# Optimization experiments

Measured on AMD Instinct MI355X. Metric: run time of the kernel, lower is better.

The kernel has to match this reference:

```python
import jax, jax.numpy as jnp
import numpy as np

N_NODES = 10000
N_EDGES = 160000
NEG_SLOPE = 0.2


def setup_inputs() -> dict:
    key = jax.random.key(0)
    ks = jax.random.split(key, 24)

    def rn(k, shape, scale):
        return (jax.random.normal(k, shape, dtype=jnp.float32) * scale)

    inp = {
        "x": rn(ks[0], (N_NODES, 128), 1.0),
        "edge_index": jax.random.randint(ks[1], (2, N_EDGES), 0, N_NODES, dtype=jnp.int32),
        "edge_attr": rn(ks[2], (N_EDGES, 8), 1.0),
        # GATConv 1: 128 -> 64 (heads=1)
        "W1": rn(ks[3], (128, 64), 0.09), "as1": rn(ks[4], (64,), 0.1), "ad1": rn(ks[5], (64,), 0.1), "b1": rn(ks[6], (64,), 0.01),
        # GATConv 2: 64 -> 256
        "W2": rn(ks[7], (64, 256), 0.125), "as2": rn(ks[8], (256,), 0.06), "ad2": rn(ks[9], (256,), 0.06), "b2": rn(ks[10], (256,), 0.01),
        # GATConv 3: 256 -> 1024
        "W3": rn(ks[11], (256, 1024), 0.0625), "as3": rn(ks[12], (1024,), 0.03), "ad3": rn(ks[13], (1024,), 0.03), "b3": rn(ks[14], (1024,), 0.01),
        # Dense head
        "lw1": rn(ks[15], (1024, 512), 0.03), "lb1": rn(ks[16], (512,), 0.01),
        "lw2": rn(ks[17], (512, 10), 0.04), "lb2": rn(ks[18], (10,), 0.01),
    }
    return inp


def gat_layer(x, src, dst, W, a_s, a_d, b, n):
    """PyG GATConv, heads=1, concat=True, add_self_loops handled by caller via src/dst."""
    h = x @ W                                   # [N, F_out]
    e = jax.nn.leaky_relu((h @ a_s)[src] + (h @ a_d)[dst], NEG_SLOPE)  # [E']
    m = jax.ops.segment_max(e, dst, num_segments=n)
    ex = jnp.exp(e - m[dst])
    denom = jax.ops.segment_sum(ex, dst, num_segments=n)
    alpha = ex / denom[dst]                     # scatter-softmax over incoming edges
    out = jax.ops.segment_sum(alpha[:, None] * h[src], dst, num_segments=n)
    return out + b


def reference(x, edge_index, edge_attr, W1, as1, ad1, b1, W2, as2, ad2, b2,
              W3, as3, ad3, b3, lw1, lb1, lw2, lb2):
    # edge_attr is accepted but ignored (GATConv built without edge_dim)
    n = x.shape[0]
    loops = jnp.arange(n, dtype=edge_index.dtype)  # add_self_loops=True
    src = jnp.concatenate([edge_index[0], loops])
    dst = jnp.concatenate([edge_index[1], loops])

    h = jax.nn.relu(gat_layer(x, src, dst, W1, as1, ad1, b1, n))
    h = jax.nn.relu(gat_layer(h, src, dst, W2, as2, ad2, b2, n))
    h = jax.nn.relu(gat_layer(h, src, dst, W3, as3, ad3, b3, n))

    pooled = jnp.max(h, axis=0, keepdims=True)  # global_max_pool, batch=None -> [1, 1024]
    z = jax.nn.relu(pooled @ lw1 + lb1)
    z = z @ lw2 + lb2
    return jax.nn.log_softmax(z, axis=1)
```

## Files before the change

kernel.cpp:

```cpp
#include <hip/hip_runtime.h>
#include <hip/hip_bf16.h>
#include <math.h>

#define NEG_SLOPE 0.2f
typedef unsigned short u16;
typedef short bf16x8 __attribute__((ext_vector_type(8)));
typedef float f32x4 __attribute__((ext_vector_type(4)));

__device__ __forceinline__ float bfu2f(u16 u) { return __uint_as_float(((unsigned)u) << 16); }
__device__ __forceinline__ u16 f2bu(float v) { return __bfloat16_as_ushort(__float2bfloat16(v)); }

__device__ __forceinline__ void gload_lds16(const void* g, void* l) {
    __builtin_amdgcn_global_load_lds((const __attribute__((address_space(1))) void*)g,
                                     (__attribute__((address_space(3))) void*)l, 16, 0, 0);
}

__global__ void prep_kernel(int* deg, int* cursor, float* pooled, int N,
                            const float* __restrict__ x, u16* __restrict__ xb,
                            const float* __restrict__ W1, u16* __restrict__ Wt1,
                            const float* __restrict__ W2, u16* __restrict__ Wt2,
                            const float* __restrict__ W3, u16* __restrict__ Wt3,
                            const float* __restrict__ as2, const float* __restrict__ ad2,
                            const float* __restrict__ as3, const float* __restrict__ ad3,
                            float* __restrict__ ws2, float* __restrict__ wd2,
                            float* __restrict__ ws3, float* __restrict__ wd3,
                            int c0, int c1, int c2, int c3, int c4) {
    int bid = blockIdx.x, tid = threadIdx.x;
    if (bid < c0) {
        int i = bid * 256 + tid;
        if (i < N) { deg[i] = 0; cursor[i] = 0; }
        if (i < 1024) pooled[i] = 0.f;
    } else if (bid < c1) {
        int i = (bid - c0) * 256 + tid;
        if (i < N * 128) xb[i] = f2bu(x[i]);
    } else if (bid < c2) {
        int i = (bid - c1) * 256 + tid;
        int k = i % 128, f = i / 128;
        Wt1[i] = f2bu(W1[k * 64 + f]);
    } else if (bid < c3) {
        int i = (bid - c2) * 256 + tid;
        int k = i % 64, f = i / 64;
        Wt2[i] = f2bu(W2[k * 256 + f]);
    } else if (bid < c4) {
        int i = (bid - c3) * 256 + tid;
        int k = i % 256, f = i / 256;
        Wt3[i] = f2bu(W3[(size_t)k * 1024 + f]);
    } else {
        int wv = ((bid - c4) * 256 + tid) >> 6;
        int lane = tid & 63;
        const float *W, *va, *vd; float *os, *od; int F, row;
        if (wv < 64) { W = W2; va = as2; vd = ad2; F = 256; row = wv; os = ws2; od = wd2; }
        else if (wv < 320) { W = W3; va = as3; vd = ad3; F = 1024; row = wv - 64; os = ws3; od = wd3; }
        else return;
        const float* wr = W + (size_t)row * F;
        float ss = 0.f, dd = 0.f;
        for (int f = lane; f < F; f += 64) { float wvv = wr[f]; ss += wvv * va[f]; dd += wvv * vd[f]; }
        for (int off = 32; off; off >>= 1) { ss += __shfl_xor(ss, off); dd += __shfl_xor(dd, off); }
        if (lane == 0) { os[row] = ss; od[row] = dd; }
    }
}

__global__ void count_kernel(const int* __restrict__ edst, int E, int N, int* deg) {
    int i = blockIdx.x * blockDim.x + threadIdx.x;
    int total = E + N;
    if (i >= total) return;
    int dn = (i < E) ? edst[i] : (i - E);
    atomicAdd(&deg[dn], 1);
}

__global__ void scan_kernel(const int* __restrict__ deg, int N, int* __restrict__ offsets) {
    __shared__ int part[257];
    int tid = threadIdx.x;
    int chunk = (N + 255) / 256;
    int begin = tid * chunk;
    int fin = begin + chunk; if (fin > N) fin = N; if (begin > N) begin = N;
    int sum = 0;
    for (int i = begin; i < fin; ++i) sum += deg[i];
    part[tid] = sum;
    __syncthreads();
    if (tid == 0) {
        int acc = 0;
        for (int t = 0; t < 256; ++t) { int v = part[t]; part[t] = acc; acc += v; }
        part[256] = acc;
    }
    __syncthreads();
    int acc = part[tid];
    for (int i = begin; i < fin; ++i) { offsets[i] = acc; acc += deg[i]; }
    if (tid == 255) offsets[N] = part[256];
}

__global__ void scatter_kernel(const int* __restrict__ esrc, const int* __restrict__ edst,
                               int E, int N, const int* __restrict__ offsets,
                               int* cursor, int* __restrict__ srcg) {
    int i = blockIdx.x * blockDim.x + threadIdx.x;
    int total = E + N;
    if (i >= total) return;
    int sn, dn;
    if (i < E) { sn = esrc[i]; dn = edst[i]; } else { sn = i - E; dn = i - E; }
    int pos = atomicAdd(&cursor[dn], 1);
    srcg[offsets[dn] + pos] = sn;
}

template <int K, int MR, bool BIASRELU, bool SD_EPI>
__global__ __launch_bounds__(256) void mfma_gemm(const u16* __restrict__ A,
                                                 const u16* __restrict__ Wt,
                                                 u16* __restrict__ C,
                                                 const float* __restrict__ bias,
                                                 int M, int F,
                                                 const float* __restrict__ asv,
                                                 const float* __restrict__ adv,
                                                 float* __restrict__ s_out,
                                                 float* __restrict__ d_out) {
    constexpr int NK = K / 32;
    int tid = threadIdx.x;
    int w = tid >> 6, l = tid & 63;
    int l15 = l & 15, q = l >> 4;
    int bm = blockIdx.x * (64 * MR);
    int bn = blockIdx.y * 64;
    int r0 = bm + w * (16 * MR);

    const u16* aptr[MR];
    int row[MR];
#pragma unroll
    for (int mr = 0; mr < MR; ++mr) {
        int r = r0 + mr * 16 + l15;
        row[mr] = r;
        int ar = (r < M) ? r : (M - 1);
        aptr[mr] = A + (size_t)ar * K + 8 * q;
    }
    const u16* bptr[4];
#pragma unroll
    for (int nt = 0; nt < 4; ++nt)
        bptr[nt] = Wt + (size_t)(bn + nt * 16 + l15) * K + 8 * q;

    f32x4 acc[MR][4];
#pragma unroll
    for (int mr = 0; mr < MR; ++mr)
#pragma unroll
        for (int nt = 0; nt < 4; ++nt) acc[mr][nt] = (f32x4){0.f, 0.f, 0.f, 0.f};

    bf16x8 a_cur[MR], b_cur[4], a_nxt[MR], b_nxt[4];
#pragma unroll
    for (int mr = 0; mr < MR; ++mr) a_cur[mr] = *(const bf16x8*)(aptr[mr]);
#pragma unroll
    for (int nt = 0; nt < 4; ++nt) b_cur[nt] = *(const bf16x8*)(bptr[nt]);

#pragma unroll
    for (int kk = 0; kk < NK; ++kk) {
        if (kk + 1 < NK) {
            int koff = (kk + 1) * 32;
#pragma unroll
            for (int mr = 0; mr < MR; ++mr) a_nxt[mr] = *(const bf16x8*)(aptr[mr] + koff);
#pragma unroll
            for (int nt = 0; nt < 4; ++nt) b_nxt[nt] = *(const bf16x8*)(bptr[nt] + koff);
        }
#pragma unroll
        for (int mr = 0; mr < MR; ++mr)
#pragma unroll
            for (int nt = 0; nt < 4; ++nt)
                acc[mr][nt] = __builtin_amdgcn_mfma_f32_16x16x32_bf16(b_cur[nt], a_cur[mr], acc[mr][nt], 0, 0, 0);
        if (kk + 1 < NK) {
#pragma unroll
            for (int mr = 0; mr < MR; ++mr) a_cur[mr] = a_nxt[mr];
#pragma unroll
            for (int nt = 0; nt < 4; ++nt) b_cur[nt] = b_nxt[nt];
        }
    }

#pragma unroll
    for (int mr = 0; mr < MR; ++mr) {
        if (row[mr] >= M) continue;
#pragma unroll
        for (int nt = 0; nt < 4; ++nt) {
            int col = bn + nt * 16 + 4 * q;
            ushort4 st;
#pragma unroll
            for (int r = 0; r < 4; ++r) {
                float v = acc[mr][nt][r];
                if (BIASRELU) { v += bias[col + r]; v = fmaxf(v, 0.f); }
                ((u16*)&st)[r] = f2bu(v);
            }
            *(ushort4*)(C + (size_t)row[mr] * F + col) = st;
        }
    }

    if constexpr (SD_EPI) {
        float ss = 0.f, dd = 0.f;
#pragma unroll
        for (int nt = 0; nt < 4; ++nt)
#pragma unroll
            for (int r = 0; r < 4; ++r) {
                int col = nt * 16 + 4 * q + r;
                float v = acc[0][nt][r];
                ss += v * asv[col];
                dd += v * adv[col];
            }
        ss += __shfl_xor(ss, 16); ss += __shfl_xor(ss, 32);
        dd += __shfl_xor(dd, 16); dd += __shfl_xor(dd, 32);
        if (q == 0 && row[0] < M) { s_out[row[0]] = ss; d_out[row[0]] = dd; }
    }
}

__global__ __launch_bounds__(512) void gemm3_kernel(const u16* __restrict__ A,
                                                    const u16* __restrict__ Wt,
                                                    const float* __restrict__ bias,
                                                    int M,
                                                    float* __restrict__ pmaxbuf) {
    constexpr int K = 256;
    constexpr int ABYTES = 128 * 512;
    __shared__ char lds[2 * ABYTES];
    int tid = threadIdx.x;
    int w = tid >> 6, lane = tid & 63;
    int w2 = w >> 2, wc = w & 3;
    int l15 = lane & 15, q = lane >> 4;
    int bid = blockIdx.x;
    int rb = bid >> 2, cbp = bid & 3;
    int bm = rb * 128;

#pragma unroll
    for (int it = 0; it < 8; ++it) {
        int c = it * 512 + tid;
        int row = c >> 5, kc = c & 31;
        int arow = bm + row; if (arow >= M) arow = M - 1;
        gload_lds16(A + (size_t)arow * K + ((kc ^ (row & 7)) * 8),
                    lds + (size_t)(it * 512 + (tid & ~63)) * 16);
    }

    const char* abase = lds;
    char* bldst = lds + ABYTES;

    for (int half = 0; half < 2; ++half) {
        if (half) __syncthreads();
        int bn = cbp * 256 + half * 128;
#pragma unroll
        for (int it = 0; it < 8; ++it) {
            int c = it * 512 + tid;
            int col = c >> 5, kc = c & 31;
            gload_lds16(Wt + (size_t)(bn + col) * K + ((kc ^ (col & 7)) * 8),
                        bldst + (size_t)(it * 512 + (tid & ~63)) * 16);
        }
        __syncthreads();

        f32x4 acc[4][2];
#pragma unroll
        for (int mr = 0; mr < 4; ++mr)
#pragma unroll
            for (int nt = 0; nt < 2; ++nt) acc[mr][nt] = (f32x4){0.f, 0.f, 0.f, 0.f};

        const char* bbase = bldst;
#pragma unroll
        for (int kk = 0; kk < 8; ++kk) {
            int c = kk * 4 + q;
            bf16x8 af[4], bfr[2];
#pragma unroll
            for (int mr = 0; mr < 4; ++mr) {
                int row = w2 * 64 + mr * 16 + l15;
                af[mr] = *(const bf16x8*)(abase + row * 512 + ((c ^ (row & 7)) * 16));
            }
#pragma unroll
            for (int nt = 0; nt < 2; ++nt) {
                int col = wc * 32 + nt * 16 + l15;
                bfr[nt] = *(const bf16x8*)(bbase + col * 512 + ((c ^ (col & 7)) * 16));
            }
#pragma unroll
            for (int mr = 0; mr < 4; ++mr)
#pragma unroll
                for (int nt = 0; nt < 2; ++nt)
                    acc[mr][nt] = __builtin_amdgcn_mfma_f32_16x16x32_bf16(bfr[nt], af[mr], acc[mr][nt], 0, 0, 0);
        }

        float pmax[2][4];
#pragma unroll
        for (int nt = 0; nt < 2; ++nt)
#pragma unroll
            for (int r = 0; r < 4; ++r) pmax[nt][r] = 0.f;
#pragma unroll
        for (int mr = 0; mr < 4; ++mr) {
            bool valid = (bm + w2 * 64 + mr * 16 + l15) < M;
#pragma unroll
            for (int nt = 0; nt < 2; ++nt)
#pragma unroll
                for (int r = 0; r < 4; ++r) {
                    float v = acc[mr][nt][r] + bias[bn + wc * 32 + nt * 16 + 4 * q + r];
                    v = fmaxf(v, 0.f);
                    if (valid) pmax[nt][r] = fmaxf(pmax[nt][r], v);
                }
        }
#pragma unroll
        for (int nt = 0; nt < 2; ++nt)
#pragma unroll
            for (int r = 0; r < 4; ++r) {
#pragma unroll
                for (int msk = 1; msk < 16; msk <<= 1)
                    pmax[nt][r] = fmaxf(pmax[nt][r], __shfl_xor(pmax[nt][r], msk));
            }
        if (l15 == 0) {
#pragma unroll
            for (int nt = 0; nt < 2; ++nt)
#pragma unroll
                for (int r = 0; r < 4; ++r)
                    pmaxbuf[(size_t)(rb * 2 + w2) * 1024 + bn + wc * 32 + nt * 16 + 4 * q + r] = pmax[nt][r];
        }
    }
}

__global__ void sd_kernel(const u16* __restrict__ h, const float* __restrict__ a_s,
                          const float* __restrict__ a_d, int N, int F,
                          float* __restrict__ s, float* __restrict__ d) {
    int wave = (blockIdx.x * blockDim.x + threadIdx.x) >> 6;
    int lane = threadIdx.x & 63;
    if (wave >= N) return;
    const u16* hrow = h + (size_t)wave * F;
    float ss = 0.f, dd = 0.f;
    for (int f = lane * 4; f < F; f += 256) {
        ushort4 u = *reinterpret_cast<const ushort4*>(hrow + f);
        float4 av = *reinterpret_cast<const float4*>(a_s + f);
        float4 dv = *reinterpret_cast<const float4*>(a_d + f);
        float h0 = bfu2f(u.x), h1 = bfu2f(u.y), h2 = bfu2f(u.z), h3 = bfu2f(u.w);
        ss += h0 * av.x + h1 * av.y + h2 * av.z + h3 * av.w;
        dd += h0 * dv.x + h1 * dv.y + h2 * dv.z + h3 * dv.w;
    }
    for (int off = 32; off; off >>= 1) { ss += __shfl_xor(ss, off); dd += __shfl_xor(dd, off); }
    if (lane == 0) { s[wave] = ss; d[wave] = dd; }
}

template <int F, int FS, bool BIASRELU, bool SD_EPI>
__global__ __launch_bounds__(256) void agg_kernel(const u16* __restrict__ h,
                                                  const float* __restrict__ sv,
                                                  const float* __restrict__ dvec,
                                                  const int* __restrict__ srcg,
                                                  const int* __restrict__ offsets,
                                                  const float* __restrict__ bias,
                                                  u16* __restrict__ out,
                                                  const float* __restrict__ wsv,
                                                  const float* __restrict__ wdv,
                                                  float* __restrict__ s_out,
                                                  float* __restrict__ d_out) {
    constexpr int FB = F / FS;
    constexpr int VPT = FB / 64;
    __shared__ float pL[256];
    __shared__ int sL[256];
    __shared__ float red[3][FB];
    int n = blockIdx.x;
    int f0 = blockIdx.y * FB;
    int tid = threadIdx.x;
    int w = tid >> 6, lane = tid & 63;
    int start = offsets[n], end = offsets[n + 1];
    int deg = end - start;
    float dval = dvec[n];
    float acc[VPT];
#pragma unroll
    for (int v = 0; v < VPT; ++v) acc[v] = 0.f;
    float inv;

    auto gpoint = [&](int sn) { return h + (size_t)sn * F + f0 + lane * VPT; };
    auto accum = [&](float pw, const u16* hp) {
        if constexpr (VPT == 4) {
            ushort4 u = *(const ushort4*)hp;
            acc[0] += pw * bfu2f(u.x); acc[1] += pw * bfu2f(u.y);
            acc[2] += pw * bfu2f(u.z); acc[3] += pw * bfu2f(u.w);
        } else if constexpr (VPT == 2) {
            ushort2 u = *(const ushort2*)hp;
            acc[0] += pw * bfu2f(u.x); acc[1] += pw * bfu2f(u.y);
        } else {
            acc[0] += pw * bfu2f(*hp);
        }
    };

    if (deg <= 256) {
        float e = -INFINITY;
        if (tid < deg) {
            int sn = srcg[start + tid];
            sL[tid] = sn;
            float v = sv[sn] + dval;
            e = (v >= 0.f) ? v : NEG_SLOPE * v;
        }
        pL[tid] = e;
        __syncthreads();
        float m = fmaxf(fmaxf(pL[lane], pL[lane + 64]), fmaxf(pL[lane + 128], pL[lane + 192]));
#pragma unroll
        for (int off2 = 32; off2; off2 >>= 1) m = fmaxf(m, __shfl_xor(m, off2));
        __syncthreads();
        float p = (tid < deg) ? expf(e - m) : 0.f;
        pL[tid] = p;
        __syncthreads();
        float t4 = (pL[lane] + pL[lane + 64]) + (pL[lane + 128] + pL[lane + 192]);
#pragma unroll
        for (int off2 = 32; off2; off2 >>= 1) t4 += __shfl_xor(t4, off2);
        inv = 1.f / t4;
        int jj = w;
        for (; jj + 4 < deg; jj += 8) {
            float p0 = pL[jj], p1 = pL[jj + 4];
            const u16* h0 = gpoint(sL[jj]);
            const u16* h1 = gpoint(sL[jj + 4]);
            accum(p0, h0);
            accum(p1, h1);
        }
        if (jj < deg) accum(pL[jj], gpoint(sL[jj]));
    } else {
        float lmax = -INFINITY;
        for (int j = start + lane; j < end; j += 64) {
            float v = sv[srcg[j]] + dval; v = (v >= 0.f) ? v : NEG_SLOPE * v;
            lmax = fmaxf(lmax, v);
        }
#pragma unroll
        for (int off2 = 32; off2; off2 >>= 1) lmax = fmaxf(lmax, __shfl_xor(lmax, off2));
        float ls = 0.f;
        for (int j = start + lane; j < end; j += 64) {
            float v = sv[srcg[j]] + dval; v = (v >= 0.f) ? v : NEG_SLOPE * v;
            ls += expf(v - lmax);
        }
#pragma unroll
        for (int off2 = 32; off2; off2 >>= 1) ls += __shfl_xor(ls, off2);
        inv = 1.f / ls;
        for (int j = start + w; j < end; j += 4) {
            int sn = srcg[j];
            float e2 = sv[sn] + dval; e2 = (e2 >= 0.f) ? e2 : NEG_SLOPE * e2;
            accum(expf(e2 - lmax), gpoint(sn));
        }
    }

    if (w > 0) {
#pragma unroll
        for (int v = 0; v < VPT; ++v) red[w - 1][lane * VPT + v] = acc[v];
    }
    __syncthreads();
    if (w != 0) return;
    float res0 = 0.f;
    if constexpr (VPT == 2) {
        ushort2 st;
#pragma unroll
        for (int v = 0; v < VPT; ++v) {
            float xv = (acc[v] + red[0][lane * 2 + v] + red[1][lane * 2 + v] + red[2][lane * 2 + v]) * inv;
            if (BIASRELU) { xv += bias[f0 + lane * 2 + v]; xv = fmaxf(xv, 0.f); }
            ((u16*)&st)[v] = f2bu(xv);
        }
        *(ushort2*)(out + (size_t)n * F + f0 + lane * 2) = st;
    } else if constexpr (VPT == 1) {
        float xv = (acc[0] + red[0][lane] + red[1][lane] + red[2][lane]) * inv;
        if (BIASRELU) { xv += bias[f0 + lane]; xv = fmaxf(xv, 0.f); }
        res0 = xv;
        out[(size_t)n * F + f0 + lane] = f2bu(xv);
    } else {
        ushort4 st;
#pragma unroll
        for (int v = 0; v < VPT; ++v) {
            float xv = (acc[v] + red[0][lane * 4 + v] + red[1][lane * 4 + v] + red[2][lane * 4 + v]) * inv;
            if (BIASRELU) { xv += bias[f0 + lane * 4 + v]; xv = fmaxf(xv, 0.f); }
            ((u16*)&st)[v] = f2bu(xv);
        }
        *(ushort4*)(out + (size_t)n * F + f0 + lane * 4) = st;
    }
    if constexpr (SD_EPI) {
        float ss = res0 * wsv[lane], dd = res0 * wdv[lane];
        for (int off2 = 32; off2; off2 >>= 1) { ss += __shfl_xor(ss, off2); dd += __shfl_xor(dd, off2); }
        if (lane == 0) { s_out[n] = ss; d_out[n] = dd; }
    }
}

__global__ void head1ap_kernel(const float* __restrict__ pmaxbuf, int nslices,
                               const float* __restrict__ lw1, float* __restrict__ part) {
    __shared__ float pk[64];
    int tid = threadIdx.x;
    int k0 = blockIdx.y * 64;
    if (tid < 64) {
        float m = 0.f;
#pragma unroll 4
        for (int s = 0; s < nslices; ++s) m = fmaxf(m, pmaxbuf[(size_t)s * 1024 + k0 + tid]);
        pk[tid] = m;
    }
    __syncthreads();
    int j = blockIdx.x * 128 + tid;
    float acc = 0.f;
#pragma unroll 8
    for (int kk = 0; kk < 64; ++kk) acc += pk[kk] * lw1[(size_t)(k0 + kk) * 512 + j];
    part[blockIdx.y * 512 + j] = acc;
}

__global__ void head1bc_kernel(const float* __restrict__ part, const float* __restrict__ lb1,
                               const float* __restrict__ lw2, const float* __restrict__ lb2,
                               float* __restrict__ out) {
    __shared__ float zs[512];
    __shared__ float z2s[10];
    int tid = threadIdx.x;
    if (tid < 512) {
        float acc = lb1[tid];
#pragma unroll
        for (int t = 0; t < 16; ++t) acc += part[t * 512 + tid];
        zs[tid] = fmaxf(acc, 0.f);
    }
    __syncthreads();
    int w = tid >> 6, lane = tid & 63;
    if (w < 10) {
        float acc = 0.f;
#pragma unroll
        for (int kc = 0; kc < 8; ++kc) {
            int k = kc * 64 + lane;
            acc += zs[k] * lw2[k * 10 + w];
        }
        for (int off = 32; off; off >>= 1) acc += __shfl_xor(acc, off);
        if (lane == 0) z2s[w] = acc + lb2[w];
    }
    __syncthreads();
    if (tid == 0) {
        float m = z2s[0];
        for (int j = 1; j < 10; ++j) m = fmaxf(m, z2s[j]);
        float ssum = 0.f;
        for (int j = 0; j < 10; ++j) ssum += expf(z2s[j] - m);
        float lse = m + logf(ssum);
        for (int j = 0; j < 10; ++j) out[j] = z2s[j] - lse;
    }
}

extern "C" void kernel_launch(void* const* d_in, const int* in_sizes, int n_in,
                              void* d_out, int out_size, void* d_ws, size_t ws_size,
                              hipStream_t stream) {
    const float* x   = (const float*)d_in[0];
    const int* ei    = (const int*)d_in[1];
    const float* W1  = (const float*)d_in[3];
    const float* as1 = (const float*)d_in[4];
    const float* ad1 = (const float*)d_in[5];
    const float* b1  = (const float*)d_in[6];
    const float* W2  = (const float*)d_in[7];
    const float* as2 = (const float*)d_in[8];
    const float* ad2 = (const float*)d_in[9];
    const float* b2  = (const float*)d_in[10];
    const float* W3  = (const float*)d_in[11];
    const float* as3 = (const float*)d_in[12];
    const float* ad3 = (const float*)d_in[13];
    const float* b3  = (const float*)d_in[14];
    const float* lw1 = (const float*)d_in[15];
    const float* lb1 = (const float*)d_in[16];
    const float* lw2 = (const float*)d_in[17];
    const float* lb2 = (const float*)d_in[18];
    float* out = (float*)d_out;

    const int N = in_sizes[0] / 128;
    const int E = in_sizes[1] / 2;
    const int total = E + N;
    const int* esrc = ei;
    const int* edst = ei + E;

    char* base = (char*)d_ws;
    size_t off = 0;
    auto alloc = [&](size_t bytes) { void* p = base + off; off = (off + bytes + 255) & ~(size_t)255; return p; };
    u16* xb    = (u16*)alloc((size_t)N * 128 * 2);
    u16* h1    = (u16*)alloc((size_t)N * 64 * 2);
    u16* a1    = (u16*)alloc((size_t)N * 64 * 2);
    u16* agg2b = (u16*)alloc((size_t)N * 64 * 2);
    u16* a2    = (u16*)alloc((size_t)N * 256 * 2);
    u16* agg3b = (u16*)alloc((size_t)N * 256 * 2);
    u16* Wt1   = (u16*)alloc(128 * 64 * 2);
    u16* Wt2   = (u16*)alloc(64 * 256 * 2);
    u16* Wt3   = (u16*)alloc(256 * 1024 * 2);
    float* ws2 = (float*)alloc(64 * 4);
    float* wd2 = (float*)alloc(64 * 4);
    float* ws3 = (float*)alloc(256 * 4);
    float* wd3 = (float*)alloc(256 * 4);
    float* sbuf = (float*)alloc((size_t)N * 4);
    float* dbuf = (float*)alloc((size_t)N * 4);
    float* pooled = (float*)alloc(1024 * 4);
    float* hpart  = (float*)alloc(16 * 512 * 4);
    int* deg     = (int*)alloc((size_t)N * 4);
    int* cursor  = (int*)alloc((size_t)N * 4);
    int* offsets = (int*)alloc((size_t)(N + 1) * 4);
    int* srcg    = (int*)alloc((size_t)total * 4);
    int nrb128g = (N + 127) / 128;
    float* pmaxbuf = (float*)alloc((size_t)nrb128g * 2 * 1024 * 4);

    const int TPB = 256;
    int gE = (total + TPB - 1) / TPB;
    int gW = (N + 3) / 4;
    int gR64 = (N + 63) / 64;
    int gR128 = (N + 127) / 128;

    int c0 = (N + 255) / 256;
    int c1 = c0 + (N * 128 + 255) / 256;
    int c2 = c1 + (128 * 64) / 256;
    int c3 = c2 + (64 * 256) / 256;
    int c4 = c3 + (256 * 1024) / 256;
    int gP = c4 + 80;
    prep_kernel<<<gP, TPB, 0, stream>>>(deg, cursor, pooled, N, x, xb,
                                        W1, Wt1, W2, Wt2, W3, Wt3,
                                        as2, ad2, as3, ad3, ws2, wd2, ws3, wd3,
                                        c0, c1, c2, c3, c4);

    count_kernel<<<gE, TPB, 0, stream>>>(edst, E, N, deg);
    scan_kernel<<<1, TPB, 0, stream>>>(deg, N, offsets);
    scatter_kernel<<<gE, TPB, 0, stream>>>(esrc, edst, E, N, offsets, cursor, srcg);

    mfma_gemm<128, 1, false, true><<<dim3(gR64, 1), TPB, 0, stream>>>(
        xb, Wt1, h1, nullptr, N, 64, as1, ad1, sbuf, dbuf);
    agg_kernel<64, 1, true, true><<<dim3(N, 1), TPB, 0, stream>>>(
        h1, sbuf, dbuf, srcg, offsets, b1, a1, ws2, wd2, sbuf, dbuf);

    agg_kernel<64, 1, false, false><<<dim3(N, 1), TPB, 0, stream>>>(
        a1, sbuf, dbuf, srcg, offsets, nullptr, agg2b, nullptr, nullptr, nullptr, nullptr);
    mfma_gemm<64, 2, true, false><<<dim3(gR128, 4), TPB, 0, stream>>>(
        agg2b, Wt2, a2, b2, N, 256, nullptr, nullptr, nullptr, nullptr);

    sd_kernel<<<gW, TPB, 0, stream>>>(a2, ws3, wd3, N, 256, sbuf, dbuf);
    agg_kernel<256, 4, false, false><<<dim3(N, 4), TPB, 0, stream>>>(
        a2, sbuf, dbuf, srcg, offsets, nullptr, agg3b, nullptr, nullptr, nullptr, nullptr);
    gemm3_kernel<<<nrb128g * 4, 512, 0, stream>>>(agg3b, Wt3, b3, N, pmaxbuf);

    head1ap_kernel<<<dim3(4, 16), 128, 0, stream>>>(pmaxbuf, nrb128g * 2, lw1, hpart);
    head1bc_kernel<<<1, 640, 0, stream>>>(hpart, lb1, lw2, lb2, out);
}
```

Before: 217.6 us.

## Split layer-3 aggregation into edge-softmax kernel and feature gather kernel

Layer-3 aggregation used to recompute the softmax attention weights in each of the four feature-slice blocks per node. A separate alpha_kernel now computes the normalized attention weights once per edge into a buffer, and gather_kernel only does the weighted feature sum with two edges per wave iteration. The agg_kernel template loses its feature-split parameter. This removes redundant exp/max work and the LDS syncs, but adds a kernel launch and an extra global round trip for the per-edge weights.

```diff
diff --git a/kernel.cpp b/kernel.cpp
--- a/kernel.cpp
+++ b/kernel.cpp
@@ -324,7 +324,82 @@
     if (lane == 0) { s[wave] = ss; d[wave] = dd; }
 }
 
-template <int F, int FS, bool BIASRELU, bool SD_EPI>
+__global__ void alpha_kernel(const float* __restrict__ sv, const float* __restrict__ dvec,
+                             const int* __restrict__ srcg, const int* __restrict__ offsets,
+                             int N, float* __restrict__ ag) {
+    int n = (blockIdx.x * blockDim.x + threadIdx.x) >> 6;
+    int lane = threadIdx.x & 63;
+    if (n >= N) return;
+    int start = offsets[n], end = offsets[n + 1];
+    float dval = dvec[n];
+    if (end - start <= 64) {
+        int j0 = start + lane;
+        float e0 = -INFINITY;
+        if (j0 < end) {
+            float v = sv[srcg[j0]] + dval;
+            e0 = (v >= 0.f) ? v : NEG_SLOPE * v;
+        }
+        float m = e0;
+#pragma unroll
+        for (int off = 32; off; off >>= 1) m = fmaxf(m, __shfl_xor(m, off));
+        float p = (j0 < end) ? expf(e0 - m) : 0.f;
+        float ls = p;
+#pragma unroll
+        for (int off = 32; off; off >>= 1) ls += __shfl_xor(ls, off);
+        if (j0 < end) ag[j0] = p / ls;
+    } else {
+        float lmax = -INFINITY;
+        for (int j = start + lane; j < end; j += 64) {
+            float v = sv[srcg[j]] + dval; v = (v >= 0.f) ? v : NEG_SLOPE * v;
+            lmax = fmaxf(lmax, v);
+        }
+#pragma unroll
+        for (int off = 32; off; off >>= 1) lmax = fmaxf(lmax, __shfl_xor(lmax, off));
+        float ls = 0.f;
+        for (int j = start + lane; j < end; j += 64) {
+            float v = sv[srcg[j]] + dval; v = (v >= 0.f) ? v : NEG_SLOPE * v;
+            ls += expf(v - lmax);
+        }
+#pragma unroll
+        for (int off = 32; off; off >>= 1) ls += __shfl_xor(ls, off);
+        float inv = 1.f / ls;
+        for (int j = start + lane; j < end; j += 64) {
+            float v = sv[srcg[j]] + dval; v = (v >= 0.f) ? v : NEG_SLOPE * v;
+            ag[j] = expf(v - lmax) * inv;
+        }
+    }
+}
+
+template <int F, int FS>
+__global__ __launch_bounds__(256) void gather_kernel(const u16* __restrict__ h,
+                                                     const float* __restrict__ ag,
+                                                     const int* __restrict__ srcg,
+                                                     const int* __restrict__ offsets,
+                                                     u16* __restrict__ out) {
+    constexpr int FB = F / FS;
+    __shared__ float red[3][FB];
+    int n = blockIdx.x;
+    int f0 = blockIdx.y * FB;
+    int tid = threadIdx.x, w = tid >> 6, lane = tid & 63;
+    int start = offsets[n], end = offsets[n + 1];
+    float acc = 0.f;
+    int j = start + w;
+    for (; j + 4 < end; j += 8) {
+        float a0 = ag[j], a1 = ag[j + 4];
+        int s0 = srcg[j], s1 = srcg[j + 4];
+        float h0 = bfu2f(h[(size_t)s0 * F + f0 + lane]);
+        float h1 = bfu2f(h[(size_t)s1 * F + f0 + lane]);
+        acc += a0 * h0 + a1 * h1;
+    }
+    if (j < end) acc += ag[j] * bfu2f(h[(size_t)srcg[j] * F + f0 + lane]);
+    if (w > 0) red[w - 1][lane] = acc;
+    __syncthreads();
+    if (w != 0) return;
+    float x = acc + red[0][lane] + red[1][lane] + red[2][lane];
+    out[(size_t)n * F + f0 + lane] = f2bu(x);
+}
+
+template <int F, bool BIASRELU, bool SD_EPI>
 __global__ __launch_bounds__(256) void agg_kernel(const u16* __restrict__ h,
                                                   const float* __restrict__ sv,
                                                   const float* __restrict__ dvec,
@@ -336,13 +411,11 @@
                                                   const float* __restrict__ wdv,
                                                   float* __restrict__ s_out,
                                                   float* __restrict__ d_out) {
-    constexpr int FB = F / FS;
-    constexpr int VPT = FB / 64;
+    constexpr int VPT = F / 64;
     __shared__ float pL[256];
     __shared__ int sL[256];
-    __shared__ float red[3][FB];
+    __shared__ float red[3][F];
     int n = blockIdx.x;
-    int f0 = blockIdx.y * FB;
     int tid = threadIdx.x;
     int w = tid >> 6, lane = tid & 63;
     int start = offsets[n], end = offsets[n + 1];
@@ -353,17 +426,13 @@
     for (int v = 0; v < VPT; ++v) acc[v] = 0.f;
     float inv;
 
-    auto gpoint = [&](int sn) { return h + (size_t)sn * F + f0 + lane * VPT; };
+    auto gpoint = [&](int sn) { return h + (size_t)sn * F + lane * VPT; };
     auto accum = [&](float pw, const u16* hp) {
-        if constexpr (VPT == 4) {
-            ushort4 u = *(const ushort4*)hp;
-            acc[0] += pw * bfu2f(u.x); acc[1] += pw * bfu2f(u.y);
-            acc[2] += pw * bfu2f(u.z); acc[3] += pw * bfu2f(u.w);
-        } else if constexpr (VPT == 2) {
+        if constexpr (VPT == 1) {
+            acc[0] += pw * bfu2f(*hp);
+        } else {
             ushort2 u = *(const ushort2*)hp;
             acc[0] += pw * bfu2f(u.x); acc[1] += pw * bfu2f(u.y);
-        } else {
-            acc[0] += pw * bfu2f(*hp);
         }
     };
 
@@ -427,29 +496,20 @@
     __syncthreads();
     if (w != 0) return;
     float res0 = 0.f;
-    if constexpr (VPT == 2) {
+    if constexpr (VPT == 1) {
+        float xv = (acc[0] + red[0][lane] + red[1][lane] + red[2][lane]) * inv;
+        if (BIASRELU) { xv += bias[lane]; xv = fmaxf(xv, 0.f); }
+        res0 = xv;
+        out[(size_t)n * F + lane] = f2bu(xv);
+    } else {
         ushort2 st;
 #pragma unroll
         for (int v = 0; v < VPT; ++v) {
             float xv = (acc[v] + red[0][lane * 2 + v] + red[1][lane * 2 + v] + red[2][lane * 2 + v]) * inv;
-            if (BIASRELU) { xv += bias[f0 + lane * 2 + v]; xv = fmaxf(xv, 0.f); }
+            if (BIASRELU) { xv += bias[lane * 2 + v]; xv = fmaxf(xv, 0.f); }
             ((u16*)&st)[v] = f2bu(xv);
         }
-        *(ushort2*)(out + (size_t)n * F + f0 + lane * 2) = st;
-    } else if constexpr (VPT == 1) {
-        float xv = (acc[0] + red[0][lane] + red[1][lane] + red[2][lane]) * inv;
-        if (BIASRELU) { xv += bias[f0 + lane]; xv = fmaxf(xv, 0.f); }
-        res0 = xv;
-        out[(size_t)n * F + f0 + lane] = f2bu(xv);
-    } else {
-        ushort4 st;
-#pragma unroll
-        for (int v = 0; v < VPT; ++v) {
-            float xv = (acc[v] + red[0][lane * 4 + v] + red[1][lane * 4 + v] + red[2][lane * 4 + v]) * inv;
-            if (BIASRELU) { xv += bias[f0 + lane * 4 + v]; xv = fmaxf(xv, 0.f); }
-            ((u16*)&st)[v] = f2bu(xv);
-        }
-        *(ushort4*)(out + (size_t)n * F + f0 + lane * 4) = st;
+        *(ushort2*)(out + (size_t)n * F + lane * 2) = st;
     }
     if constexpr (SD_EPI) {
         float ss = res0 * wsv[lane], dd = res0 * wdv[lane];
@@ -559,6 +619,7 @@
     float* wd3 = (float*)alloc(256 * 4);
     float* sbuf = (float*)alloc((size_t)N * 4);
     float* dbuf = (float*)alloc((size_t)N * 4);
+    float* ag   = (float*)alloc((size_t)total * 4);
     float* pooled = (float*)alloc(1024 * 4);
     float* hpart  = (float*)alloc(16 * 512 * 4);
     int* deg     = (int*)alloc((size_t)N * 4);
@@ -591,17 +652,17 @@
 
     mfma_gemm<128, 1, false, true><<<dim3(gR64, 1), TPB, 0, stream>>>(
         xb, Wt1, h1, nullptr, N, 64, as1, ad1, sbuf, dbuf);
-    agg_kernel<64, 1, true, true><<<dim3(N, 1), TPB, 0, stream>>>(
+    agg_kernel<64, true, true><<<N, TPB, 0, stream>>>(
         h1, sbuf, dbuf, srcg, offsets, b1, a1, ws2, wd2, sbuf, dbuf);
 
-    agg_kernel<64, 1, false, false><<<dim3(N, 1), TPB, 0, stream>>>(
+    agg_kernel<64, false, false><<<N, TPB, 0, stream>>>(
         a1, sbuf, dbuf, srcg, offsets, nullptr, agg2b, nullptr, nullptr, nullptr, nullptr);
     mfma_gemm<64, 2, true, false><<<dim3(gR128, 4), TPB, 0, stream>>>(
         agg2b, Wt2, a2, b2, N, 256, nullptr, nullptr, nullptr, nullptr);
 
     sd_kernel<<<gW, TPB, 0, stream>>>(a2, ws3, wd3, N, 256, sbuf, dbuf);
-    agg_kernel<256, 4, false, false><<<dim3(N, 4), TPB, 0, stream>>>(
-        a2, sbuf, dbuf, srcg, offsets, nullptr, agg3b, nullptr, nullptr, nullptr, nullptr);
+    alpha_kernel<<<gW, TPB, 0, stream>>>(sbuf, dbuf, srcg, offsets, N, ag);
+    gather_kernel<256, 4><<<dim3(N, 4), TPB, 0, stream>>>(a2, ag, srcg, offsets, agg3b);
     gemm3_kernel<<<nrb128g * 4, 512, 0, stream>>>(agg3b, Wt3, b3, N, pmaxbuf);
 
     head1ap_kernel<<<dim3(4, 16), 128, 0, stream>>>(pmaxbuf, nrb128g * 2, lw1, hpart);
```

Result: faster. 210.3 us (-3.3%).
